# Kernel tuning notes

Measured on AMD Instinct MI355X. Metric: run time of the kernel, lower is better.

## Reference

```python
import jax, jax.numpy as jnp
import numpy as np

ROPE_BASE = 1024.0
EPS = 1e-6

def _rms_norm(x):
    return x / jnp.sqrt(jnp.mean(x * x, axis=-1, keepdims=True) + EPS)

def _rotary_tables(T, head_dim):
    steps = head_dim // 4
    inv_freq = (1.0 / ROPE_BASE) ** jnp.linspace(0.0, 1.0, steps, dtype=jnp.float32)
    inv_freq = jnp.concatenate([inv_freq, jnp.zeros(steps, dtype=jnp.float32)])  # [head_dim//2]
    theta = jnp.arange(T, dtype=jnp.float32)[:, None] * inv_freq[None, :]  # [T, head_dim//2]
    return jnp.cos(theta), jnp.sin(theta)

def _apply_rotary(x, cos, sin):
    # x: [B,H,T,hd]; cos/sin: [T, hd//2]
    d = x.shape[-1] // 2
    x1, x2 = x[..., :d], x[..., d:]
    return jnp.concatenate([x1 * cos + x2 * sin, -x1 * sin + x2 * cos], axis=-1)

def setup_inputs() -> dict:
    key = jax.random.key(0)
    ks = jax.random.split(key, 5)
    B, T, C = 4, 2048, 1024
    return {
        "x": jax.random.normal(ks[0], (B, T, C), dtype=jnp.float32),
        "v1": jax.random.normal(ks[1], (B, T, C), dtype=jnp.float32),
        "qkv_weight": 0.02 * jax.random.normal(ks[2], (3, C, C), dtype=jnp.float32),
        "c_proj_w": 0.02 * jax.random.normal(ks[3], (C, C), dtype=jnp.float32),
        "c_proj_b": jnp.zeros((C,), dtype=jnp.float32),
        "lamb": jnp.full((1,), 0.5, dtype=jnp.float32),
        "attn_window": 512,
    }

def reference(x, v1, qkv_weight, c_proj_w, c_proj_b, lamb, attn_window):
    B, T, C = x.shape
    H = 16
    hd = C // H
    # fused QKV projection: qkv_weight is [3, C, C], applied as x @ W_k^T
    qkv = jnp.einsum('btc,kdc->kbtd', x, qkv_weight)  # [3,B,T,C]
    q, k, v = qkv[0], qkv[1], qkv[2]
    def to_heads(t):
        return t.reshape(B, T, H, hd).transpose(0, 2, 1, 3)  # [B,H,T,hd]
    query, key_, value = to_heads(q), to_heads(k), to_heads(v)
    v1h = to_heads(v1)
    lam = lamb[0]
    value = (1.0 - lam) * value + lam * v1h  # value-residual blend
    query = _rms_norm(query)
    key_ = _rms_norm(key_)
    cos, sin = _rotary_tables(T, hd)
    query = _apply_rotary(query, cos, sin)
    key_ = _apply_rotary(key_, cos, sin)
    # windowed causal mask: attend iff 0 <= i - j < attn_window
    i = jnp.arange(T)[:, None]
    j = jnp.arange(T)[None, :]
    allowed = (i - j < attn_window) & (j <= i)
    bias = jnp.where(allowed, 0.0, -jnp.inf).astype(x.dtype)  # [T,T]
    scale = 1.0 / jnp.sqrt(jnp.asarray(hd, dtype=x.dtype))
    scores = jnp.einsum('bhtd,bhsd->bhts', query, key_) * scale + bias
    attn = jax.nn.softmax(scores, axis=-1)
    out = jnp.einsum('bhts,bhsd->bhtd', attn, value)  # [B,H,T,hd]
    out = out.transpose(0, 2, 1, 3).reshape(B, T, C)
    y = out @ c_proj_w.T + c_proj_b
    return (y, value)
```

## Files before the change

### kernel.cpp

```cpp
#include <hip/hip_runtime.h>
#include <stdint.h>

typedef __attribute__((ext_vector_type(8))) short short8;
typedef __attribute__((ext_vector_type(4))) float f32x4;

#define LDS_AS __attribute__((address_space(3)))
#define GLOB_AS __attribute__((address_space(1)))

__device__ __forceinline__ void gload_lds16(const void* g, void* l) {
    __builtin_amdgcn_global_load_lds((const GLOB_AS uint32_t*)g,
                                     (LDS_AS uint32_t*)l, 16, 0, 0);
}

__device__ __forceinline__ unsigned short f2bf(float f) {
    uint32_t u = __builtin_bit_cast(uint32_t, f);
    u += 0x7fffu + ((u >> 16) & 1u);
    return (unsigned short)(u >> 16);
}
__device__ __forceinline__ float bf2f(unsigned short u) {
    uint32_t v = ((uint32_t)u) << 16;
    return __builtin_bit_cast(float, v);
}

__global__ void cvt_kernel(const float* __restrict__ src,
                           unsigned short* __restrict__ dst, int n) {
    int i = (blockIdx.x * blockDim.x + threadIdx.x) * 4;
    if (i < n) {
        float4 v = *(const float4*)(src + i);
        ushort4 o;
        o.x = f2bf(v.x); o.y = f2bf(v.y); o.z = f2bf(v.z); o.w = f2bf(v.w);
        *(ushort4*)(dst + i) = o;
    }
}

__global__ void rope_tables(float* __restrict__ cosT, float* __restrict__ sinT) {
    int tid = blockIdx.x * blockDim.x + threadIdx.x;
    int t = tid >> 5, i = tid & 31;
    float f = (i < 16) ? exp2f(-10.0f * (float)i / 15.0f) : 0.0f;
    float th = (float)t * f;
    cosT[tid] = cosf(th);
    sinT[tid] = sinf(th);
}

template <int MODE>
__global__ __launch_bounds__(256, 3) void gemm_bt(
    const unsigned short* __restrict__ A, const unsigned short* __restrict__ B,
    int K,
    unsigned short* __restrict__ qbuf, unsigned short* __restrict__ kbuf,
    float* __restrict__ vout, unsigned short* __restrict__ vbT,
    const float* __restrict__ v1, const float* __restrict__ lambp,
    float* __restrict__ y, const float* __restrict__ bias,
    const float* __restrict__ cosT, const float* __restrict__ sinT)
{
    __shared__ unsigned short As[2][128 * 32];
    __shared__ unsigned short Bs[2][128 * 32];
    const int tid = threadIdx.x;
    const int lane = tid & 63, w = tid >> 6;
    const int wr = w >> 1, wc = w & 1;
    const int lr = lane & 15, lh = lane >> 4;
    const long m0 = (long)blockIdx.x * 128;
    const long n0 = (long)blockIdx.y * 128;

    const int row0 = w * 16 + (lane >> 2);
    const int colb = (lane & 3) * 16;
    const char* pa0 = (const char*)A + ((m0 + row0) * (long)K) * 2 + colb;
    const char* pa1 = pa0 + 64 * (long)K * 2;
    const char* pb0 = (const char*)B + ((n0 + row0) * (long)K) * 2 + colb;
    const char* pb1 = pb0 + 64 * (long)K * 2;
    char* la = (char*)&As[0][0] + w * 1024;
    char* lb = (char*)&Bs[0][0] + w * 1024;
    const int BUF = 128 * 32 * 2;

    f32x4 acc[4][4] = {};

    auto STAGE = [&](int bo) {
        gload_lds16(pa0, la + bo);
        gload_lds16(pa1, la + bo + 4096);
        gload_lds16(pb0, lb + bo);
        gload_lds16(pb1, lb + bo + 4096);
        pa0 += 64; pa1 += 64; pb0 += 64; pb1 += 64;
    };
    auto COMPUTE = [&](int bo) {
        const unsigned short* as = (const unsigned short*)((const char*)&As[0][0] + bo);
        const unsigned short* bs = (const unsigned short*)((const char*)&Bs[0][0] + bo);
        short8 a[4], b[4];
        #pragma unroll
        for (int i = 0; i < 4; ++i)
            a[i] = *(const short8*)&as[(wr * 64 + i * 16 + lr) * 32 + lh * 8];
        #pragma unroll
        for (int i = 0; i < 4; ++i)
            b[i] = *(const short8*)&bs[(wc * 64 + i * 16 + lr) * 32 + lh * 8];
        #pragma unroll
        for (int i = 0; i < 4; ++i)
            #pragma unroll
            for (int j = 0; j < 4; ++j)
                acc[i][j] = __builtin_amdgcn_mfma_f32_16x16x32_bf16(
                    a[i], b[j], acc[i][j], 0, 0, 0);
    };

    STAGE(0);
    __syncthreads();
    for (int k0 = 0; k0 < K; k0 += 64) {
        STAGE(BUF);
        COMPUTE(0);
        __syncthreads();
        if (k0 + 64 < K) STAGE(0);
        COMPUTE(BUF);
        __syncthreads();
    }

    if constexpr (MODE == 1) {
        const long nbase = n0 + wc * 64;
        const int kk = (int)(nbase >> 10);
        const int h = (int)((nbase & 1023) >> 6);
        if (kk == 2) {
            float lam = lambp[0];
            #pragma unroll
            for (int i = 0; i < 4; ++i)
            #pragma unroll
            for (int j = 0; j < 4; ++j)
            #pragma unroll
            for (int r = 0; r < 4; ++r) {
                long m = m0 + wr * 64 + i * 16 + lh * 4 + r;
                int d = j * 16 + lr;
                int rem = h * 64 + d;
                long b_ = m >> 11, t = m & 2047;
                size_t idx = (((size_t)(b_ * 16 + h)) * 2048 + t) * 64 + d;
                float vv = v1[(size_t)m * 1024 + rem];
                float val = (1.0f - lam) * acc[i][j][r] + lam * vv;
                vout[idx] = val;
                vbT[(((size_t)(b_ * 16 + h)) * 64 + d) * 2048 + t] = f2bf(val);
            }
        } else {
            unsigned short* dst = (kk == 0) ? qbuf : kbuf;
            #pragma unroll
            for (int i = 0; i < 4; ++i)
            #pragma unroll
            for (int r = 0; r < 4; ++r) {
                float v0 = acc[i][0][r], v1_ = acc[i][1][r];
                float v2 = acc[i][2][r], v3 = acc[i][3][r];
                float ss = v0 * v0 + v1_ * v1_ + v2 * v2 + v3 * v3;
                ss += __shfl_xor(ss, 1);
                ss += __shfl_xor(ss, 2);
                ss += __shfl_xor(ss, 4);
                ss += __shfl_xor(ss, 8);
                float inv = rsqrtf(ss * (1.0f / 64.0f) + 1e-6f);
                float x0 = v0 * inv, x1 = v1_ * inv;
                float x2 = v2 * inv, x3 = v3 * inv;
                long m = m0 + wr * 64 + i * 16 + lh * 4 + r;
                int t = (int)(m & 2047);
                long b_ = m >> 11;
                float c0 = cosT[t * 32 + lr],      s0 = sinT[t * 32 + lr];
                float c1 = cosT[t * 32 + 16 + lr], s1 = sinT[t * 32 + 16 + lr];
                size_t rb = (((size_t)(b_ * 16 + h)) * 2048 + t) * 64;
                dst[rb + 0 * 16 + lr] = f2bf( x0 * c0 + x2 * s0);
                dst[rb + 1 * 16 + lr] = f2bf( x1 * c1 + x3 * s1);
                dst[rb + 2 * 16 + lr] = f2bf(-x0 * s0 + x2 * c0);
                dst[rb + 3 * 16 + lr] = f2bf(-x1 * s1 + x3 * c1);
            }
        }
    } else {
        #pragma unroll
        for (int i = 0; i < 4; ++i)
        #pragma unroll
        for (int j = 0; j < 4; ++j)
        #pragma unroll
        for (int r = 0; r < 4; ++r) {
            long m = m0 + wr * 64 + i * 16 + lh * 4 + r;
            long n = n0 + wc * 64 + j * 16 + lr;
            y[(size_t)m * 1024 + n] = acc[i][j][r] + bias[n];
        }
    }
}

__global__ __launch_bounds__(512, 2) void attn_kernel(
    const unsigned short* __restrict__ qn, const unsigned short* __restrict__ kn,
    const unsigned short* __restrict__ vtb, unsigned short* __restrict__ attn_out,
    const int* __restrict__ winp)
{
    __shared__ unsigned short Ks[2][64 * 64];
    __shared__ unsigned short Vt[2][64 * 64];
    __shared__ unsigned short Pl[8][16 * 72];
    const int tid = threadIdx.x, lane = tid & 63, w = tid >> 6;
    const int lr = lane & 15, lh = lane >> 4;
    const int bh = blockIdx.x;
    const int qt2 = blockIdx.y;
    const int t0 = qt2 * 128;
    const int win = winp[0];
    const int qrow = t0 + w * 16;

    short8 qf[2];
    #pragma unroll
    for (int ks = 0; ks < 2; ++ks)
        qf[ks] = *(const short8*)&qn[((size_t)bh * 2048 + qrow + lr) * 64 + ks * 32 + lh * 8];

    const int srow = tid >> 3;
    const int scol = (tid & 7) ^ (srow & 7);
    const char* kg = (const char*)kn + ((size_t)bh * 2048 + srow) * 128 + scol * 16;
    const char* vg = (const char*)vtb + ((size_t)(bh * 64 + srow)) * 4096 + scol * 16;
    char* lk = (char*)&Ks[0][0] + w * 1024;
    char* lv = (char*)&Vt[0][0] + w * 1024;

    auto STAGE = [&](int buf, int j0) {
        gload_lds16(kg + (size_t)j0 * 128, lk + buf * 8192);
        gload_lds16(vg + (size_t)j0 * 2,   lv + buf * 8192);
    };

    f32x4 oacc[4] = {};
    float mrow[4], lrow[4];
    #pragma unroll
    for (int r = 0; r < 4; ++r) { mrow[r] = -1e30f; lrow[r] = 0.f; }

    const float C = 0.125f * 1.44269504f;
    const int kvt0 = max(0, t0 - win + 1) >> 6;
    const int kvt1 = (t0 + 127) >> 6;

    STAGE(0, kvt0 * 64);
    __syncthreads();
    for (int kvt = kvt0; kvt <= kvt1; ++kvt) {
        const int j0 = kvt * 64;
        const int buf = (kvt - kvt0) & 1;
        if (kvt < kvt1) STAGE(buf ^ 1, j0 + 64);

        if (j0 <= qrow + 15 && j0 + 63 >= qrow + 16 - win) {
            const char* ksb = (const char*)&Ks[buf][0];
            const char* vtb_ = (const char*)&Vt[buf][0];

            float sv[4][4];
            #pragma unroll
            for (int kt = 0; kt < 4; ++kt) {
                f32x4 s = {};
                #pragma unroll
                for (int ks = 0; ks < 2; ++ks) {
                    int row = kt * 16 + lr;
                    int off = row * 128 + (((ks * 4 + lh) ^ (row & 7)) * 16);
                    short8 kf = *(const short8*)(ksb + off);
                    s = __builtin_amdgcn_mfma_f32_16x16x32_bf16(qf[ks], kf, s, 0, 0, 0);
                }
                #pragma unroll
                for (int r = 0; r < 4; ++r) {
                    int qi = qrow + lh * 4 + r;
                    int ji = j0 + kt * 16 + lr;
                    bool ok = (ji <= qi) && (qi - ji < win);
                    sv[kt][r] = ok ? s[r] * C : -1e30f;
                }
            }

            float pn[4][4];
            #pragma unroll
            for (int r = 0; r < 4; ++r) {
                float tm = fmaxf(fmaxf(sv[0][r], sv[1][r]), fmaxf(sv[2][r], sv[3][r]));
                #pragma unroll
                for (int m = 1; m < 16; m <<= 1) tm = fmaxf(tm, __shfl_xor(tm, m));
                float nm = fmaxf(mrow[r], tm);
                float alpha = exp2f(mrow[r] - nm);
                float ps = 0.f;
                #pragma unroll
                for (int kt = 0; kt < 4; ++kt) {
                    float p = exp2f(sv[kt][r] - nm);
                    pn[kt][r] = p; ps += p;
                }
                #pragma unroll
                for (int m = 1; m < 16; m <<= 1) ps += __shfl_xor(ps, m);
                lrow[r] = lrow[r] * alpha + ps;
                mrow[r] = nm;
                #pragma unroll
                for (int dt = 0; dt < 4; ++dt) oacc[dt][r] *= alpha;
            }

            #pragma unroll
            for (int kt = 0; kt < 4; ++kt)
                #pragma unroll
                for (int r = 0; r < 4; ++r)
                    Pl[w][(lh * 4 + r) * 72 + kt * 16 + lr] = f2bf(pn[kt][r]);

            short8 pf[2];
            #pragma unroll
            for (int ks = 0; ks < 2; ++ks)
                pf[ks] = *(const short8*)&Pl[w][lr * 72 + ks * 32 + lh * 8];
            #pragma unroll
            for (int dt = 0; dt < 4; ++dt)
                #pragma unroll
                for (int ks = 0; ks < 2; ++ks) {
                    int row = dt * 16 + lr;
                    int off = row * 128 + (((ks * 4 + lh) ^ (row & 7)) * 16);
                    short8 vf = *(const short8*)(vtb_ + off);
                    oacc[dt] = __builtin_amdgcn_mfma_f32_16x16x32_bf16(pf[ks], vf, oacc[dt], 0, 0, 0);
                }
        }
        __syncthreads();
    }

    int b = bh >> 4, h = bh & 15;
    #pragma unroll
    for (int dt = 0; dt < 4; ++dt)
        #pragma unroll
        for (int r = 0; r < 4; ++r) {
            int t = qrow + lh * 4 + r;
            float o = oacc[dt][r] / lrow[r];
            attn_out[((size_t)b * 2048 + t) * 1024 + h * 64 + dt * 16 + lr] = f2bf(o);
        }
}

extern "C" void kernel_launch(void* const* d_in, const int* in_sizes, int n_in,
                              void* d_out, int out_size, void* d_ws, size_t ws_size,
                              hipStream_t stream) {
    const float* x    = (const float*)d_in[0];
    const float* v1   = (const float*)d_in[1];
    const float* qkvw = (const float*)d_in[2];
    const float* cpw  = (const float*)d_in[3];
    const float* cpb  = (const float*)d_in[4];
    const float* lamb = (const float*)d_in[5];
    const int*   winp = (const int*)d_in[6];

    float* y    = (float*)d_out;
    float* vout = y + (size_t)8192 * 1024;

    unsigned short* vbT = (unsigned short*)y;

    char* ws = (char*)d_ws;
    unsigned short* xb   = (unsigned short*)(ws);
    unsigned short* Wb   = (unsigned short*)(ws + (16u << 20));
    unsigned short* Wp   = (unsigned short*)(ws + (22u << 20));
    unsigned short* qbuf = (unsigned short*)(ws + (24u << 20));
    unsigned short* kbuf = (unsigned short*)(ws + (40u << 20));
    float* cosT = (float*)(ws + (56u << 20));
    float* sinT = (float*)(ws + (56u << 20) + (256u << 10));

    cvt_kernel<<<8388608 / 1024, 256, 0, stream>>>(x, xb, 8388608);
    cvt_kernel<<<3145728 / 1024, 256, 0, stream>>>(qkvw, Wb, 3145728);
    cvt_kernel<<<1048576 / 1024, 256, 0, stream>>>(cpw, Wp, 1048576);
    rope_tables<<<65536 / 256, 256, 0, stream>>>(cosT, sinT);

    gemm_bt<1><<<dim3(64, 24), 256, 0, stream>>>(xb, Wb, 1024,
        qbuf, kbuf, vout, vbT, v1, lamb, nullptr, nullptr, cosT, sinT);

    attn_kernel<<<dim3(64, 16), 512, 0, stream>>>(qbuf, kbuf, vbT, xb, winp);

    gemm_bt<2><<<dim3(64, 8), 256, 0, stream>>>(xb, Wp, 1024,
        nullptr, nullptr, nullptr, nullptr, nullptr, nullptr, y, cpb, nullptr, nullptr);
}
```

Baseline: 202.3 us.

## Rewrite projection GEMMs as 256x128-tile, 8-wave, triple-buffered swizzled-LDS kernels

Replaces the 128x128, 4-wave double-buffered bf16 GEMM used for both the QKV and output projections with a 256x128 tile computed by 8 waves. It uses 64-wide K steps and three LDS stages, filled by direct global-to-LDS loads and tracked with explicit vmcnt waits. The LDS layout is XOR-swizzled to avoid bank conflicts. Loads for later stages are split into two halves and interleaved with the MFMA phases, with s_setprio raising priority during the math. The goal is more operand reuse per byte loaded and better overlap of memory with MFMA work. In exchange, the 144KB of LDS limits each CU to one block, and the grid has fewer blocks.

```diff
diff --git a/kernel.cpp b/kernel.cpp
--- a/kernel.cpp
+++ b/kernel.cpp
@@ -43,7 +43,7 @@
 }
 
 template <int MODE>
-__global__ __launch_bounds__(256, 3) void gemm_bt(
+__global__ __launch_bounds__(512, 2) void gemm8p(
     const unsigned short* __restrict__ A, const unsigned short* __restrict__ B,
     int K,
     unsigned short* __restrict__ qbuf, unsigned short* __restrict__ kbuf,
@@ -52,61 +52,116 @@
     float* __restrict__ y, const float* __restrict__ bias,
     const float* __restrict__ cosT, const float* __restrict__ sinT)
 {
-    __shared__ unsigned short As[2][128 * 32];
-    __shared__ unsigned short Bs[2][128 * 32];
-    const int tid = threadIdx.x;
-    const int lane = tid & 63, w = tid >> 6;
+    __shared__ __align__(16) char smem[147456];
+    char* const AL = smem;
+    char* const BL = smem + 98304;
+    const int tid = threadIdx.x, lane = tid & 63, w = tid >> 6;
     const int wr = w >> 1, wc = w & 1;
     const int lr = lane & 15, lh = lane >> 4;
-    const long m0 = (long)blockIdx.x * 128;
+    const long m0 = (long)blockIdx.x * 256;
     const long n0 = (long)blockIdx.y * 128;
-
-    const int row0 = w * 16 + (lane >> 2);
-    const int colb = (lane & 3) * 16;
-    const char* pa0 = (const char*)A + ((m0 + row0) * (long)K) * 2 + colb;
-    const char* pa1 = pa0 + 64 * (long)K * 2;
-    const char* pb0 = (const char*)B + ((n0 + row0) * (long)K) * 2 + colb;
-    const char* pb1 = pb0 + 64 * (long)K * 2;
-    char* la = (char*)&As[0][0] + w * 1024;
-    char* lb = (char*)&Bs[0][0] + w * 1024;
-    const int BUF = 128 * 32 * 2;
+    const int NT = K >> 6;
+
+    const int srow = tid >> 3;
+    const int swc  = (tid & 7) ^ (srow & 7);
+    const long rsb = (long)K * 2;
+    const char* pa0 = (const char*)A + (m0 + srow +   0) * rsb + swc * 16;
+    const char* pa1 = (const char*)A + (m0 + srow +  64) * rsb + swc * 16;
+    const char* pa2 = (const char*)A + (m0 + srow + 128) * rsb + swc * 16;
+    const char* pa3 = (const char*)A + (m0 + srow + 192) * rsb + swc * 16;
+    const char* pb0 = (const char*)B + (n0 + srow +   0) * rsb + swc * 16;
+    const char* pb1 = (const char*)B + (n0 + srow +  64) * rsb + swc * 16;
+    char* const lA = AL + w * 1024;
+    char* const lB = BL + w * 1024;
+
+    auto STAGE_A3 = [&](int aoff, int boff) {
+        gload_lds16(pa0, lA + aoff);
+        gload_lds16(pa1, lA + aoff + 8192);
+        gload_lds16(pb0, lB + boff);
+    };
+    auto STAGE_B3 = [&](int aoff, int boff) {
+        gload_lds16(pa2, lA + aoff + 16384);
+        gload_lds16(pa3, lA + aoff + 24576);
+        gload_lds16(pb1, lB + boff + 8192);
+        pa0 += 128; pa1 += 128; pa2 += 128; pa3 += 128;
+        pb0 += 128; pb1 += 128;
+    };
+
+    const int arow_b = (wr * 64 + lr) * 128;
+    const int brow_b = (wc * 64 + lr) * 128;
+    const int x0 = ((lh)     ^ (lr & 7)) * 16;
+    const int x1 = ((4 + lh) ^ (lr & 7)) * 16;
 
     f32x4 acc[4][4] = {};
 
-    auto STAGE = [&](int bo) {
-        gload_lds16(pa0, la + bo);
-        gload_lds16(pa1, la + bo + 4096);
-        gload_lds16(pb0, lb + bo);
-        gload_lds16(pb1, lb + bo + 4096);
-        pa0 += 64; pa1 += 64; pb0 += 64; pb1 += 64;
-    };
-    auto COMPUTE = [&](int bo) {
-        const unsigned short* as = (const unsigned short*)((const char*)&As[0][0] + bo);
-        const unsigned short* bs = (const unsigned short*)((const char*)&Bs[0][0] + bo);
-        short8 a[4], b[4];
-        #pragma unroll
-        for (int i = 0; i < 4; ++i)
-            a[i] = *(const short8*)&as[(wr * 64 + i * 16 + lr) * 32 + lh * 8];
-        #pragma unroll
-        for (int i = 0; i < 4; ++i)
-            b[i] = *(const short8*)&bs[(wc * 64 + i * 16 + lr) * 32 + lh * 8];
-        #pragma unroll
-        for (int i = 0; i < 4; ++i)
-            #pragma unroll
-            for (int j = 0; j < 4; ++j)
-                acc[i][j] = __builtin_amdgcn_mfma_f32_16x16x32_bf16(
-                    a[i], b[j], acc[i][j], 0, 0, 0);
-    };
-
-    STAGE(0);
-    __syncthreads();
-    for (int k0 = 0; k0 < K; k0 += 64) {
-        STAGE(BUF);
-        COMPUTE(0);
-        __syncthreads();
-        if (k0 + 64 < K) STAGE(0);
-        COMPUTE(BUF);
-        __syncthreads();
+    STAGE_A3(0, 0);           STAGE_B3(0, 0);
+    STAGE_A3(32768, 16384);   STAGE_B3(32768, 16384);
+
+    int cA = 0, cB = 0;
+    int sA = 65536, sB = 32768;
+
+    for (int t = 0; t < NT; ++t) {
+        if (t < NT - 1) asm volatile("s_waitcnt vmcnt(6)" ::: "memory");
+        else            asm volatile("s_waitcnt vmcnt(0)" ::: "memory");
+        __builtin_amdgcn_s_barrier();
+        __builtin_amdgcn_sched_barrier(0);
+
+        const char* ab = AL + cA;
+        const char* bb = BL + cB;
+        const bool st = (t < NT - 2);
+
+        short8 bfr[4][2], afr[2][2];
+        #pragma unroll
+        for (int ni = 0; ni < 4; ++ni) {
+            bfr[ni][0] = *(const short8*)(bb + brow_b + ni * 2048 + x0);
+            bfr[ni][1] = *(const short8*)(bb + brow_b + ni * 2048 + x1);
+        }
+        #pragma unroll
+        for (int mi = 0; mi < 2; ++mi) {
+            afr[mi][0] = *(const short8*)(ab + arow_b + mi * 2048 + x0);
+            afr[mi][1] = *(const short8*)(ab + arow_b + mi * 2048 + x1);
+        }
+        if (st) STAGE_A3(sA, sB);
+        __builtin_amdgcn_s_barrier();
+        asm volatile("s_waitcnt lgkmcnt(0)" ::: "memory");
+        __builtin_amdgcn_sched_barrier(0);
+        __builtin_amdgcn_s_setprio(1);
+        #pragma unroll
+        for (int mi = 0; mi < 2; ++mi)
+            #pragma unroll
+            for (int ni = 0; ni < 4; ++ni)
+                #pragma unroll
+                for (int ks = 0; ks < 2; ++ks)
+                    acc[mi][ni] = __builtin_amdgcn_mfma_f32_16x16x32_bf16(
+                        afr[mi][ks], bfr[ni][ks], acc[mi][ni], 0, 0, 0);
+        __builtin_amdgcn_s_setprio(0);
+        __builtin_amdgcn_s_barrier();
+
+        short8 afr2[2][2];
+        #pragma unroll
+        for (int mi = 0; mi < 2; ++mi) {
+            afr2[mi][0] = *(const short8*)(ab + arow_b + (mi + 2) * 2048 + x0);
+            afr2[mi][1] = *(const short8*)(ab + arow_b + (mi + 2) * 2048 + x1);
+        }
+        if (st) STAGE_B3(sA, sB);
+        __builtin_amdgcn_s_barrier();
+        asm volatile("s_waitcnt lgkmcnt(0)" ::: "memory");
+        __builtin_amdgcn_sched_barrier(0);
+        __builtin_amdgcn_s_setprio(1);
+        #pragma unroll
+        for (int mi = 0; mi < 2; ++mi)
+            #pragma unroll
+            for (int ni = 0; ni < 4; ++ni)
+                #pragma unroll
+                for (int ks = 0; ks < 2; ++ks)
+                    acc[mi + 2][ni] = __builtin_amdgcn_mfma_f32_16x16x32_bf16(
+                        afr2[mi][ks], bfr[ni][ks], acc[mi + 2][ni], 0, 0, 0);
+        __builtin_amdgcn_s_setprio(0);
+
+        cA = (cA == 65536) ? 0 : cA + 32768;
+        cB = (cB == 32768) ? 0 : cB + 16384;
+        sA = (sA == 65536) ? 0 : sA + 32768;
+        sB = (sB == 32768) ? 0 : sB + 16384;
     }
 
     if constexpr (MODE == 1) {
@@ -145,18 +200,18 @@
                 ss += __shfl_xor(ss, 4);
                 ss += __shfl_xor(ss, 8);
                 float inv = rsqrtf(ss * (1.0f / 64.0f) + 1e-6f);
-                float x0 = v0 * inv, x1 = v1_ * inv;
-                float x2 = v2 * inv, x3 = v3 * inv;
+                float x0f = v0 * inv, x1f = v1_ * inv;
+                float x2f = v2 * inv, x3f = v3 * inv;
                 long m = m0 + wr * 64 + i * 16 + lh * 4 + r;
                 int t = (int)(m & 2047);
                 long b_ = m >> 11;
                 float c0 = cosT[t * 32 + lr],      s0 = sinT[t * 32 + lr];
                 float c1 = cosT[t * 32 + 16 + lr], s1 = sinT[t * 32 + 16 + lr];
                 size_t rb = (((size_t)(b_ * 16 + h)) * 2048 + t) * 64;
-                dst[rb + 0 * 16 + lr] = f2bf( x0 * c0 + x2 * s0);
-                dst[rb + 1 * 16 + lr] = f2bf( x1 * c1 + x3 * s1);
-                dst[rb + 2 * 16 + lr] = f2bf(-x0 * s0 + x2 * c0);
-                dst[rb + 3 * 16 + lr] = f2bf(-x1 * s1 + x3 * c1);
+                dst[rb + 0 * 16 + lr] = f2bf( x0f * c0 + x2f * s0);
+                dst[rb + 1 * 16 + lr] = f2bf( x1f * c1 + x3f * s1);
+                dst[rb + 2 * 16 + lr] = f2bf(-x0f * s0 + x2f * c0);
+                dst[rb + 3 * 16 + lr] = f2bf(-x1f * s1 + x3f * c1);
             }
         }
     } else {
@@ -332,11 +387,11 @@
     cvt_kernel<<<1048576 / 1024, 256, 0, stream>>>(cpw, Wp, 1048576);
     rope_tables<<<65536 / 256, 256, 0, stream>>>(cosT, sinT);
 
-    gemm_bt<1><<<dim3(64, 24), 256, 0, stream>>>(xb, Wb, 1024,
+    gemm8p<1><<<dim3(32, 24), 512, 0, stream>>>(xb, Wb, 1024,
         qbuf, kbuf, vout, vbT, v1, lamb, nullptr, nullptr, cosT, sinT);
 
     attn_kernel<<<dim3(64, 16), 512, 0, stream>>>(qbuf, kbuf, vbT, xb, winp);
 
-    gemm_bt<2><<<dim3(64, 8), 256, 0, stream>>>(xb, Wp, 1024,
+    gemm8p<2><<<dim3(32, 8), 512, 0, stream>>>(xb, Wp, 1024,
         nullptr, nullptr, nullptr, nullptr, nullptr, nullptr, y, cpb, nullptr, nullptr);
 }
```

Result: faster. 188.2 us (-7.0%).

## Enlarge GEMM tiles to 256-row blocks with explicit waitcnt-pipelined double buffering

Applied to the files above, without the earlier changes.

Replaces the 128x128 GEMM with a 512-thread kernel using 256-row tiles (256 columns for QKV, 128 for the output projection). It splits each 64-wide K step into two halves staged asynchronously with manual vmcnt/barrier control and raises wave priority around the MFMA bursts. The aim is more data reuse per LDS load and better overlap of global loads with compute. The cost is more registers per thread and fewer blocks in the grid, which may leave CUs underfilled, especially for the output projection with 256 blocks.

```diff
diff --git a/kernel.cpp b/kernel.cpp
--- a/kernel.cpp
+++ b/kernel.cpp
@@ -21,6 +21,11 @@
     uint32_t v = ((uint32_t)u) << 16;
     return __builtin_bit_cast(float, v);
 }
+
+#define WAIT_VM(N)   asm volatile("s_waitcnt vmcnt(" #N ")" ::: "memory")
+#define WAIT_LGKM0() asm volatile("s_waitcnt lgkmcnt(0)" ::: "memory")
+#define BAR()        asm volatile("s_barrier" ::: "memory")
+#define FENCE()      __builtin_amdgcn_sched_barrier(0)
 
 __global__ void cvt_kernel(const float* __restrict__ src,
                            unsigned short* __restrict__ dst, int n) {
@@ -42,8 +47,8 @@
     sinT[tid] = sinf(th);
 }
 
-template <int MODE>
-__global__ __launch_bounds__(256, 3) void gemm_bt(
+template <int MODE, int NJ>
+__global__ __launch_bounds__(512, 2) void gemm_kp(
     const unsigned short* __restrict__ A, const unsigned short* __restrict__ B,
     int K,
     unsigned short* __restrict__ qbuf, unsigned short* __restrict__ kbuf,
@@ -52,61 +57,95 @@
     float* __restrict__ y, const float* __restrict__ bias,
     const float* __restrict__ cosT, const float* __restrict__ sinT)
 {
-    __shared__ unsigned short As[2][128 * 32];
-    __shared__ unsigned short Bs[2][128 * 32];
-    const int tid = threadIdx.x;
-    const int lane = tid & 63, w = tid >> 6;
-    const int wr = w >> 1, wc = w & 1;
+    constexpr int ASZ = 32768;
+    constexpr int BHALF = NJ * 4096;
+    constexpr int STRIDE = ASZ + 2 * BHALF;
+    __shared__ __align__(16) char smem[2 * STRIDE];
+
+    const int tid = threadIdx.x, lane = tid & 63, w = tid >> 6;
+    const int wr = w >> 2, wc = w & 3;
     const int lr = lane & 15, lh = lane >> 4;
-    const long m0 = (long)blockIdx.x * 128;
-    const long n0 = (long)blockIdx.y * 128;
-
-    const int row0 = w * 16 + (lane >> 2);
-    const int colb = (lane & 3) * 16;
-    const char* pa0 = (const char*)A + ((m0 + row0) * (long)K) * 2 + colb;
-    const char* pa1 = pa0 + 64 * (long)K * 2;
-    const char* pb0 = (const char*)B + ((n0 + row0) * (long)K) * 2 + colb;
-    const char* pb1 = pb0 + 64 * (long)K * 2;
-    char* la = (char*)&As[0][0] + w * 1024;
-    char* lb = (char*)&Bs[0][0] + w * 1024;
-    const int BUF = 128 * 32 * 2;
-
-    f32x4 acc[4][4] = {};
-
-    auto STAGE = [&](int bo) {
-        gload_lds16(pa0, la + bo);
-        gload_lds16(pa1, la + bo + 4096);
-        gload_lds16(pb0, lb + bo);
-        gload_lds16(pb1, lb + bo + 4096);
-        pa0 += 64; pa1 += 64; pb0 += 64; pb1 += 64;
+    const long m0 = (long)blockIdx.x * 256;
+    const long n0 = (long)blockIdx.y * (NJ * 64);
+    const int NT = K >> 6;
+    const long rsb = (long)K * 2;
+
+    const int srow = w * 16 + lr;
+    const char* pa0 = (const char*)A + (m0 + srow) * rsb + lh * 16;
+    const char* pa1 = pa0 + 128 * rsb;
+    const char* pb0 = (const char*)B + (n0 + srow) * rsb + lh * 16;
+    const char* pb1 = pb0 + 128 * rsb;
+
+    auto STAGE_U = [&](int bufsel, int kh) {
+        char* ab = smem + bufsel * STRIDE + kh * 16384;
+        char* bb = smem + bufsel * STRIDE + ASZ + kh * BHALF;
+        gload_lds16(pa0 + kh * 64, ab + (w + 0) * 1024);
+        gload_lds16(pa1 + kh * 64, ab + (w + 8) * 1024);
+        gload_lds16(pb0 + kh * 64, bb + (w + 0) * 1024);
+        if constexpr (NJ == 4)
+            gload_lds16(pb1 + kh * 64, bb + (w + 8) * 1024);
     };
-    auto COMPUTE = [&](int bo) {
-        const unsigned short* as = (const unsigned short*)((const char*)&As[0][0] + bo);
-        const unsigned short* bs = (const unsigned short*)((const char*)&Bs[0][0] + bo);
-        short8 a[4], b[4];
-        #pragma unroll
-        for (int i = 0; i < 4; ++i)
-            a[i] = *(const short8*)&as[(wr * 64 + i * 16 + lr) * 32 + lh * 8];
-        #pragma unroll
-        for (int i = 0; i < 4; ++i)
-            b[i] = *(const short8*)&bs[(wc * 64 + i * 16 + lr) * 32 + lh * 8];
-        #pragma unroll
-        for (int i = 0; i < 4; ++i)
-            #pragma unroll
-            for (int j = 0; j < 4; ++j)
-                acc[i][j] = __builtin_amdgcn_mfma_f32_16x16x32_bf16(
-                    a[i], b[j], acc[i][j], 0, 0, 0);
-    };
-
-    STAGE(0);
-    __syncthreads();
-    for (int k0 = 0; k0 < K; k0 += 64) {
-        STAGE(BUF);
-        COMPUTE(0);
-        __syncthreads();
-        if (k0 + 64 < K) STAGE(0);
-        COMPUTE(BUF);
-        __syncthreads();
+
+    const int fofs = lh * 256 + lr * 16;
+
+    f32x4 acc[8][NJ] = {};
+
+    STAGE_U(0, 0);
+    STAGE_U(0, 1);
+    pa0 += 128; pa1 += 128; pb0 += 128; pb1 += 128;
+
+    for (int t = 0; t < NT; ++t) {
+        const int buf = t & 1, nbuf = buf ^ 1;
+        const bool st = (t + 1 < NT);
+        const char* ab = smem + buf * STRIDE;
+        const char* bb = ab + ASZ;
+
+        if constexpr (NJ == 4) WAIT_VM(4); else WAIT_VM(3);
+        BAR();
+        FENCE();
+        if (st) STAGE_U(nbuf, 0);
+        short8 af[8], bf[NJ];
+        #pragma unroll
+        for (int mi = 0; mi < 8; ++mi)
+            af[mi] = *(const short8*)(ab + (wr * 8 + mi) * 1024 + fofs);
+        #pragma unroll
+        for (int nj = 0; nj < NJ; ++nj)
+            bf[nj] = *(const short8*)(bb + (wc * NJ + nj) * 1024 + fofs);
+        WAIT_LGKM0();
+        FENCE();
+        __builtin_amdgcn_s_setprio(1);
+        #pragma unroll
+        for (int mi = 0; mi < 8; ++mi)
+            #pragma unroll
+            for (int nj = 0; nj < NJ; ++nj)
+                acc[mi][nj] = __builtin_amdgcn_mfma_f32_16x16x32_bf16(
+                    af[mi], bf[nj], acc[mi][nj], 0, 0, 0);
+        __builtin_amdgcn_s_setprio(0);
+
+        if (st) { if constexpr (NJ == 4) WAIT_VM(4); else WAIT_VM(3); }
+        else    WAIT_VM(0);
+        BAR();
+        FENCE();
+        if (st) {
+            STAGE_U(nbuf, 1);
+            pa0 += 128; pa1 += 128; pb0 += 128; pb1 += 128;
+        }
+        #pragma unroll
+        for (int mi = 0; mi < 8; ++mi)
+            af[mi] = *(const short8*)(ab + 16384 + (wr * 8 + mi) * 1024 + fofs);
+        #pragma unroll
+        for (int nj = 0; nj < NJ; ++nj)
+            bf[nj] = *(const short8*)(bb + BHALF + (wc * NJ + nj) * 1024 + fofs);
+        WAIT_LGKM0();
+        FENCE();
+        __builtin_amdgcn_s_setprio(1);
+        #pragma unroll
+        for (int mi = 0; mi < 8; ++mi)
+            #pragma unroll
+            for (int nj = 0; nj < NJ; ++nj)
+                acc[mi][nj] = __builtin_amdgcn_mfma_f32_16x16x32_bf16(
+                    af[mi], bf[nj], acc[mi][nj], 0, 0, 0);
+        __builtin_amdgcn_s_setprio(0);
     }
 
     if constexpr (MODE == 1) {
@@ -116,12 +155,12 @@
         if (kk == 2) {
             float lam = lambp[0];
             #pragma unroll
-            for (int i = 0; i < 4; ++i)
+            for (int i = 0; i < 8; ++i)
             #pragma unroll
             for (int j = 0; j < 4; ++j)
             #pragma unroll
             for (int r = 0; r < 4; ++r) {
-                long m = m0 + wr * 64 + i * 16 + lh * 4 + r;
+                long m = m0 + wr * 128 + i * 16 + lh * 4 + r;
                 int d = j * 16 + lr;
                 int rem = h * 64 + d;
                 long b_ = m >> 11, t = m & 2047;
@@ -134,7 +173,7 @@
         } else {
             unsigned short* dst = (kk == 0) ? qbuf : kbuf;
             #pragma unroll
-            for (int i = 0; i < 4; ++i)
+            for (int i = 0; i < 8; ++i)
             #pragma unroll
             for (int r = 0; r < 4; ++r) {
                 float v0 = acc[i][0][r], v1_ = acc[i][1][r];
@@ -145,29 +184,29 @@
                 ss += __shfl_xor(ss, 4);
                 ss += __shfl_xor(ss, 8);
                 float inv = rsqrtf(ss * (1.0f / 64.0f) + 1e-6f);
-                float x0 = v0 * inv, x1 = v1_ * inv;
-                float x2 = v2 * inv, x3 = v3 * inv;
-                long m = m0 + wr * 64 + i * 16 + lh * 4 + r;
+                float x0f = v0 * inv, x1f = v1_ * inv;
+                float x2f = v2 * inv, x3f = v3 * inv;
+                long m = m0 + wr * 128 + i * 16 + lh * 4 + r;
                 int t = (int)(m & 2047);
                 long b_ = m >> 11;
                 float c0 = cosT[t * 32 + lr],      s0 = sinT[t * 32 + lr];
                 float c1 = cosT[t * 32 + 16 + lr], s1 = sinT[t * 32 + 16 + lr];
                 size_t rb = (((size_t)(b_ * 16 + h)) * 2048 + t) * 64;
-                dst[rb + 0 * 16 + lr] = f2bf( x0 * c0 + x2 * s0);
-                dst[rb + 1 * 16 + lr] = f2bf( x1 * c1 + x3 * s1);
-                dst[rb + 2 * 16 + lr] = f2bf(-x0 * s0 + x2 * c0);
-                dst[rb + 3 * 16 + lr] = f2bf(-x1 * s1 + x3 * c1);
+                dst[rb + 0 * 16 + lr] = f2bf( x0f * c0 + x2f * s0);
+                dst[rb + 1 * 16 + lr] = f2bf( x1f * c1 + x3f * s1);
+                dst[rb + 2 * 16 + lr] = f2bf(-x0f * s0 + x2f * c0);
+                dst[rb + 3 * 16 + lr] = f2bf(-x1f * s1 + x3f * c1);
             }
         }
     } else {
         #pragma unroll
-        for (int i = 0; i < 4; ++i)
-        #pragma unroll
-        for (int j = 0; j < 4; ++j)
+        for (int i = 0; i < 8; ++i)
+        #pragma unroll
+        for (int j = 0; j < NJ; ++j)
         #pragma unroll
         for (int r = 0; r < 4; ++r) {
-            long m = m0 + wr * 64 + i * 16 + lh * 4 + r;
-            long n = n0 + wc * 64 + j * 16 + lr;
+            long m = m0 + wr * 128 + i * 16 + lh * 4 + r;
+            long n = n0 + wc * (NJ * 16) + j * 16 + lr;
             y[(size_t)m * 1024 + n] = acc[i][j][r] + bias[n];
         }
     }
@@ -332,11 +371,11 @@
     cvt_kernel<<<1048576 / 1024, 256, 0, stream>>>(cpw, Wp, 1048576);
     rope_tables<<<65536 / 256, 256, 0, stream>>>(cosT, sinT);
 
-    gemm_bt<1><<<dim3(64, 24), 256, 0, stream>>>(xb, Wb, 1024,
+    gemm_kp<1, 4><<<dim3(32, 12), 512, 0, stream>>>(xb, Wb, 1024,
         qbuf, kbuf, vout, vbT, v1, lamb, nullptr, nullptr, cosT, sinT);
 
     attn_kernel<<<dim3(64, 16), 512, 0, stream>>>(qbuf, kbuf, vbT, xb, winp);
 
-    gemm_bt<2><<<dim3(64, 8), 256, 0, stream>>>(xb, Wp, 1024,
+    gemm_kp<2, 2><<<dim3(32, 8), 512, 0, stream>>>(xb, Wp, 1024,
         nullptr, nullptr, nullptr, nullptr, nullptr, nullptr, y, cpb, nullptr, nullptr);
 }
```

New measurement: 224.0 us. 1.11x slower.

## Triple-buffer GEMM K-loop with vmcnt waits and merge conversion kernels

Applied to the files above, without the earlier changes.

The GEMM main loop changes from a double-buffered scheme with two __syncthreads per step to a three-slot ring buffer. It prefetches two tiles ahead, waits on vmcnt counts with a single barrier per 32-wide K step, and raises wave priority around the MFMA block. The LDS layout is also changed so each 16x32 fragment sits in its own contiguous 1 KB block, which may reduce bank conflicts. The three fp32-to-bf16 conversion launches are merged into one kernel to save launch overhead. The cost is more LDS per block (48 KB) and hand-placed waitcnt logic that has to match the number of loads in flight.

```diff
diff --git a/kernel.cpp b/kernel.cpp
--- a/kernel.cpp
+++ b/kernel.cpp
@@ -22,15 +22,26 @@
     return __builtin_bit_cast(float, v);
 }
 
-__global__ void cvt_kernel(const float* __restrict__ src,
-                           unsigned short* __restrict__ dst, int n) {
-    int i = (blockIdx.x * blockDim.x + threadIdx.x) * 4;
-    if (i < n) {
-        float4 v = *(const float4*)(src + i);
-        ushort4 o;
-        o.x = f2bf(v.x); o.y = f2bf(v.y); o.z = f2bf(v.z); o.w = f2bf(v.w);
-        *(ushort4*)(dst + i) = o;
-    }
+#define WAIT_VM(N)   asm volatile("s_waitcnt vmcnt(" #N ")" ::: "memory")
+#define WAIT_LGKM0() asm volatile("s_waitcnt lgkmcnt(0)" ::: "memory")
+#define BAR()        asm volatile("s_barrier" ::: "memory")
+#define FENCE()      __builtin_amdgcn_sched_barrier(0)
+
+__global__ void cvt3_kernel(const float* __restrict__ s0,
+                            const float* __restrict__ s1,
+                            const float* __restrict__ s2,
+                            unsigned short* __restrict__ d0,
+                            unsigned short* __restrict__ d1,
+                            unsigned short* __restrict__ d2) {
+    long e = ((long)blockIdx.x * blockDim.x + threadIdx.x) * 4;
+    const float* s; unsigned short* d; long off;
+    if (e < 8388608)        { s = s0; d = d0; off = e; }
+    else if (e < 11534336)  { s = s1; d = d1; off = e - 8388608; }
+    else                    { s = s2; d = d2; off = e - 11534336; }
+    float4 v = *(const float4*)(s + off);
+    ushort4 o;
+    o.x = f2bf(v.x); o.y = f2bf(v.y); o.z = f2bf(v.z); o.w = f2bf(v.w);
+    *(ushort4*)(d + off) = o;
 }
 
 __global__ void rope_tables(float* __restrict__ cosT, float* __restrict__ sinT) {
@@ -43,7 +54,7 @@
 }
 
 template <int MODE>
-__global__ __launch_bounds__(256, 3) void gemm_bt(
+__global__ __launch_bounds__(256, 3) void gemm128(
     const unsigned short* __restrict__ A, const unsigned short* __restrict__ B,
     int K,
     unsigned short* __restrict__ qbuf, unsigned short* __restrict__ kbuf,
@@ -52,61 +63,65 @@
     float* __restrict__ y, const float* __restrict__ bias,
     const float* __restrict__ cosT, const float* __restrict__ sinT)
 {
-    __shared__ unsigned short As[2][128 * 32];
-    __shared__ unsigned short Bs[2][128 * 32];
-    const int tid = threadIdx.x;
-    const int lane = tid & 63, w = tid >> 6;
+    __shared__ __align__(16) char smem[49152];
+    const int tid = threadIdx.x, lane = tid & 63, w = tid >> 6;
     const int wr = w >> 1, wc = w & 1;
     const int lr = lane & 15, lh = lane >> 4;
     const long m0 = (long)blockIdx.x * 128;
     const long n0 = (long)blockIdx.y * 128;
-
-    const int row0 = w * 16 + (lane >> 2);
-    const int colb = (lane & 3) * 16;
-    const char* pa0 = (const char*)A + ((m0 + row0) * (long)K) * 2 + colb;
-    const char* pa1 = pa0 + 64 * (long)K * 2;
-    const char* pb0 = (const char*)B + ((n0 + row0) * (long)K) * 2 + colb;
-    const char* pb1 = pb0 + 64 * (long)K * 2;
-    char* la = (char*)&As[0][0] + w * 1024;
-    char* lb = (char*)&Bs[0][0] + w * 1024;
-    const int BUF = 128 * 32 * 2;
-
-    f32x4 acc[4][4] = {};
-
-    auto STAGE = [&](int bo) {
-        gload_lds16(pa0, la + bo);
-        gload_lds16(pa1, la + bo + 4096);
-        gload_lds16(pb0, lb + bo);
-        gload_lds16(pb1, lb + bo + 4096);
+    const int NT = K >> 5;
+    const long rsb = (long)K * 2;
+
+    const char* pa0 = (const char*)A + (m0 + w * 16 + lr) * rsb + lh * 16;
+    const char* pa1 = pa0 + 64 * rsb;
+    const char* pb0 = (const char*)B + (n0 + w * 16 + lr) * rsb + lh * 16;
+    const char* pb1 = pb0 + 64 * rsb;
+
+    auto STAGE = [&](int slot) {
+        char* d = smem + slot;
+        gload_lds16(pa0, d + w * 1024);
+        gload_lds16(pa1, d + 4096 + w * 1024);
+        gload_lds16(pb0, d + 8192 + w * 1024);
+        gload_lds16(pb1, d + 12288 + w * 1024);
         pa0 += 64; pa1 += 64; pb0 += 64; pb1 += 64;
     };
-    auto COMPUTE = [&](int bo) {
-        const unsigned short* as = (const unsigned short*)((const char*)&As[0][0] + bo);
-        const unsigned short* bs = (const unsigned short*)((const char*)&Bs[0][0] + bo);
-        short8 a[4], b[4];
-        #pragma unroll
-        for (int i = 0; i < 4; ++i)
-            a[i] = *(const short8*)&as[(wr * 64 + i * 16 + lr) * 32 + lh * 8];
-        #pragma unroll
-        for (int i = 0; i < 4; ++i)
-            b[i] = *(const short8*)&bs[(wc * 64 + i * 16 + lr) * 32 + lh * 8];
-        #pragma unroll
-        for (int i = 0; i < 4; ++i)
-            #pragma unroll
-            for (int j = 0; j < 4; ++j)
-                acc[i][j] = __builtin_amdgcn_mfma_f32_16x16x32_bf16(
-                    a[i], b[j], acc[i][j], 0, 0, 0);
-    };
+
+    const int fofs = lh * 256 + lr * 16;
+
+    f32x4 acc[4][4] = {};
 
     STAGE(0);
-    __syncthreads();
-    for (int k0 = 0; k0 < K; k0 += 64) {
-        STAGE(BUF);
-        COMPUTE(0);
-        __syncthreads();
-        if (k0 + 64 < K) STAGE(0);
-        COMPUTE(BUF);
-        __syncthreads();
+    STAGE(16384);
+
+    int cs = 0, ss = 32768;
+    for (int t = 0; t < NT; ++t) {
+        if (t < NT - 1) WAIT_VM(4);
+        else            WAIT_VM(0);
+        BAR();
+        FENCE();
+        if (t + 2 < NT) STAGE(ss);
+
+        const char* cb = smem + cs;
+        short8 af[4], bf[4];
+        #pragma unroll
+        for (int mi = 0; mi < 4; ++mi)
+            af[mi] = *(const short8*)(cb + (wr * 4 + mi) * 1024 + fofs);
+        #pragma unroll
+        for (int nj = 0; nj < 4; ++nj)
+            bf[nj] = *(const short8*)(cb + 8192 + (wc * 4 + nj) * 1024 + fofs);
+        WAIT_LGKM0();
+        FENCE();
+        __builtin_amdgcn_s_setprio(1);
+        #pragma unroll
+        for (int mi = 0; mi < 4; ++mi)
+            #pragma unroll
+            for (int nj = 0; nj < 4; ++nj)
+                acc[mi][nj] = __builtin_amdgcn_mfma_f32_16x16x32_bf16(
+                    af[mi], bf[nj], acc[mi][nj], 0, 0, 0);
+        __builtin_amdgcn_s_setprio(0);
+
+        cs = (cs == 32768) ? 0 : cs + 16384;
+        ss = (ss == 32768) ? 0 : ss + 16384;
     }
 
     if constexpr (MODE == 1) {
@@ -139,24 +154,24 @@
             for (int r = 0; r < 4; ++r) {
                 float v0 = acc[i][0][r], v1_ = acc[i][1][r];
                 float v2 = acc[i][2][r], v3 = acc[i][3][r];
-                float ss = v0 * v0 + v1_ * v1_ + v2 * v2 + v3 * v3;
-                ss += __shfl_xor(ss, 1);
-                ss += __shfl_xor(ss, 2);
-                ss += __shfl_xor(ss, 4);
-                ss += __shfl_xor(ss, 8);
-                float inv = rsqrtf(ss * (1.0f / 64.0f) + 1e-6f);
-                float x0 = v0 * inv, x1 = v1_ * inv;
-                float x2 = v2 * inv, x3 = v3 * inv;
+                float ss_ = v0 * v0 + v1_ * v1_ + v2 * v2 + v3 * v3;
+                ss_ += __shfl_xor(ss_, 1);
+                ss_ += __shfl_xor(ss_, 2);
+                ss_ += __shfl_xor(ss_, 4);
+                ss_ += __shfl_xor(ss_, 8);
+                float inv = rsqrtf(ss_ * (1.0f / 64.0f) + 1e-6f);
+                float x0f = v0 * inv, x1f = v1_ * inv;
+                float x2f = v2 * inv, x3f = v3 * inv;
                 long m = m0 + wr * 64 + i * 16 + lh * 4 + r;
                 int t = (int)(m & 2047);
                 long b_ = m >> 11;
                 float c0 = cosT[t * 32 + lr],      s0 = sinT[t * 32 + lr];
                 float c1 = cosT[t * 32 + 16 + lr], s1 = sinT[t * 32 + 16 + lr];
                 size_t rb = (((size_t)(b_ * 16 + h)) * 2048 + t) * 64;
-                dst[rb + 0 * 16 + lr] = f2bf( x0 * c0 + x2 * s0);
-                dst[rb + 1 * 16 + lr] = f2bf( x1 * c1 + x3 * s1);
-                dst[rb + 2 * 16 + lr] = f2bf(-x0 * s0 + x2 * c0);
-                dst[rb + 3 * 16 + lr] = f2bf(-x1 * s1 + x3 * c1);
+                dst[rb + 0 * 16 + lr] = f2bf( x0f * c0 + x2f * s0);
+                dst[rb + 1 * 16 + lr] = f2bf( x1f * c1 + x3f * s1);
+                dst[rb + 2 * 16 + lr] = f2bf(-x0f * s0 + x2f * c0);
+                dst[rb + 3 * 16 + lr] = f2bf(-x1f * s1 + x3f * c1);
             }
         }
     } else {
@@ -327,16 +342,14 @@
     float* cosT = (float*)(ws + (56u << 20));
     float* sinT = (float*)(ws + (56u << 20) + (256u << 10));
 
-    cvt_kernel<<<8388608 / 1024, 256, 0, stream>>>(x, xb, 8388608);
-    cvt_kernel<<<3145728 / 1024, 256, 0, stream>>>(qkvw, Wb, 3145728);
-    cvt_kernel<<<1048576 / 1024, 256, 0, stream>>>(cpw, Wp, 1048576);
+    cvt3_kernel<<<12288, 256, 0, stream>>>(x, qkvw, cpw, xb, Wb, Wp);
     rope_tables<<<65536 / 256, 256, 0, stream>>>(cosT, sinT);
 
-    gemm_bt<1><<<dim3(64, 24), 256, 0, stream>>>(xb, Wb, 1024,
+    gemm128<1><<<dim3(64, 24), 256, 0, stream>>>(xb, Wb, 1024,
         qbuf, kbuf, vout, vbT, v1, lamb, nullptr, nullptr, cosT, sinT);
 
     attn_kernel<<<dim3(64, 16), 512, 0, stream>>>(qbuf, kbuf, vbT, xb, winp);
 
-    gemm_bt<2><<<dim3(64, 8), 256, 0, stream>>>(xb, Wp, 1024,
+    gemm128<2><<<dim3(64, 8), 256, 0, stream>>>(xb, Wp, 1024,
         nullptr, nullptr, nullptr, nullptr, nullptr, nullptr, y, cpb, nullptr, nullptr);
 }
```

After: 232.1 us. 1.15x slower.
